# Kernel optimization log

Hardware: AMD Instinct MI355X
Metric: run time of the kernel (lower is better)

## Reference

```python
import jax, jax.numpy as jnp
import numpy as np

DIM, NH, WS, SS, MLP_RATIO = 192, 6, 8, 4, 4
EPS = 1e-5


def _rel_pos_index(ws):
    coords = np.stack(np.meshgrid(np.arange(ws), np.arange(ws), indexing='ij')).reshape(2, -1)
    rel = (coords[:, :, None] - coords[:, None, :]).transpose(1, 2, 0)
    rel[:, :, 0] += ws - 1
    rel[:, :, 1] += ws - 1
    rel[:, :, 0] *= 2 * ws - 1
    return rel.sum(-1)  # (ws*ws, ws*ws) int


def _attn_mask(hp, wp, ws, ss):
    img = np.zeros((hp, wp))
    slices = (slice(0, -ws), slice(-ws, -ss), slice(-ss, None))
    cnt = 0
    for hs in slices:
        for vs in slices:
            img[hs, vs] = cnt
            cnt += 1
    mw = img.reshape(hp // ws, ws, wp // ws, ws).transpose(0, 2, 1, 3).reshape(-1, ws * ws)
    am = mw[:, None, :] - mw[:, :, None]  # (nW, N, N)
    return jnp.asarray(np.where(am != 0, -100.0, 0.0).astype(np.float32))


def _ln(x, g, b):
    mu = jnp.mean(x, axis=-1, keepdims=True)
    var = jnp.mean(jnp.square(x - mu), axis=-1, keepdims=True)
    return (x - mu) * jax.lax.rsqrt(var + EPS) * g + b


def setup_inputs():
    key = jax.random.key(0)
    ks = jax.random.split(key, 8)
    B, H, W, C = 8, 128, 128, DIM
    hid = C * MLP_RATIO
    n = lambda k, s: jax.random.normal(k, s, dtype=jnp.float32) * 0.02
    return {
        'x': jax.random.normal(ks[0], (B, H * W, C), dtype=jnp.float32),
        'h': H, 'w': W,
        'norm1_g': jnp.ones((C,), jnp.float32), 'norm1_b': jnp.zeros((C,), jnp.float32),
        'qkv_w': n(ks[1], (C, 3 * C)), 'qkv_b': jnp.zeros((3 * C,), jnp.float32),
        'proj_w': n(ks[2], (C, C)), 'proj_b': jnp.zeros((C,), jnp.float32),
        'rel_bias_table': n(ks[3], ((2 * WS - 1) ** 2, NH)),
        'norm2_g': jnp.ones((C,), jnp.float32), 'norm2_b': jnp.zeros((C,), jnp.float32),
        'fc1_w': n(ks[4], (C, hid)), 'fc1_b': jnp.zeros((hid,), jnp.float32),
        'fc2_w': n(ks[5], (hid, C)), 'fc2_b': jnp.zeros((C,), jnp.float32),
    }


def reference(x, h, w, norm1_g, norm1_b, qkv_w, qkv_b, proj_w, proj_b,
              rel_bias_table, norm2_g, norm2_b, fc1_w, fc1_b, fc2_w, fc2_b):
    B, L, C = x.shape
    ws, ss, nh = WS, SS, NH
    hd = C // nh
    scale = hd ** (-0.5)

    shortcut = x
    xg = _ln(x, norm1_g, norm1_b).reshape(B, h, w, C)

    pad_h = (-h) % ws
    pad_w = (-w) % ws
    if pad_h or pad_w:
        xg = jnp.pad(xg, ((0, 0), (0, pad_h), (0, pad_w), (0, 0)))
    hp, wp = h + pad_h, w + pad_w
    if ss > 0:
        xg = jnp.roll(xg, (-ss, -ss), axis=(1, 2))

    # window partition -> (nB, N, C)
    win = xg.reshape(B, hp // ws, ws, wp // ws, ws, C).transpose(0, 1, 3, 2, 4, 5).reshape(-1, ws * ws, C)
    nB, N, _ = win.shape

    qkv = (win @ qkv_w + qkv_b).reshape(nB, N, 3, nh, hd).transpose(2, 0, 3, 1, 4)
    q, k, v = qkv[0] * scale, qkv[1], qkv[2]  # (nB, nh, N, hd)

    attn = jnp.einsum('bhnd,bhmd->bhnm', q, k)  # (nB, nh, N, N)
    rpi = _rel_pos_index(ws)
    bias = rel_bias_table[rpi.reshape(-1)].reshape(N, N, nh).transpose(2, 0, 1)
    attn = attn + bias[None]
    if ss > 0:
        mask = _attn_mask(hp, wp, ws, ss)  # (nW, N, N)
        nW = mask.shape[0]
        attn = (attn.reshape(nB // nW, nW, nh, N, N) + mask[None, :, None]).reshape(nB, nh, N, N)
    attn = jax.nn.softmax(attn, axis=-1)

    out = jnp.einsum('bhnm,bhmd->bnhd', attn, v).reshape(nB, N, C)
    out = out @ proj_w + proj_b

    # window reverse
    out = out.reshape(B, hp // ws, wp // ws, ws, ws, C).transpose(0, 1, 3, 2, 4, 5).reshape(B, hp, wp, C)
    if ss > 0:
        out = jnp.roll(out, (ss, ss), axis=(1, 2))
    out = out[:, :h, :w].reshape(B, h * w, C)

    x = shortcut + out
    xn2 = _ln(x, norm2_g, norm2_b)
    mlp = jax.nn.gelu(xn2 @ fc1_w + fc1_b, approximate=False) @ fc2_w + fc2_b
    return x + mlp
```

## Files before the change

kernel.cpp:

```cpp
#include <hip/hip_runtime.h>

typedef unsigned short u16;
typedef unsigned int   u32;
typedef __attribute__((ext_vector_type(8))) short bf16x8;
typedef __attribute__((ext_vector_type(4))) float f32x4;

#define L_TOK   16384
#define C_DIM   192
#define HID_DIM 768

#define OFF_QKV  0
#define OFF_PROJ 110592
#define OFF_FC1  147456
#define OFF_FC2  294912
#define CVT_TOT  442368

union FragU { int4 i4; bf16x8 h8; };

#define MFMA_B16(a,b,c) __builtin_amdgcn_mfma_f32_16x16x32_bf16(a,b,c,0,0,0)

__device__ __forceinline__ u16 f2bf(float f) {
    u32 t; __builtin_memcpy(&t, &f, 4);
    t += 0x7FFFu + ((t >> 16) & 1u);
    return (u16)(t >> 16);
}

__global__ __launch_bounds__(256) void k_cvt(
    const float* __restrict__ qkvw, const float* __restrict__ projw,
    const float* __restrict__ fc1w, const float* __restrict__ fc2w,
    u16* __restrict__ ws)
{
    const int i = blockIdx.x * 256 + threadIdx.x;
    if (i >= CVT_TOT) return;
    float v; int dst;
    if (i < OFF_PROJ) {
        const int k = i / 576, col = i % 576;
        const int grp = col / 192, rem = col % 192;
        const int head = rem >> 5, dim = rem & 31;
        v = qkvw[i];
        dst = OFF_QKV + head * (96 * 192) + (grp * 32 + dim) * 192 + k;
    } else if (i < OFF_FC1) {
        const int s = i - OFF_PROJ;
        const int cin = s / 192, cout = s % 192;
        const int head = cin >> 5, j = cin & 31;
        v = projw[s];
        dst = OFF_PROJ + head * (192 * 32) + cout * 32 + j;
    } else if (i < OFF_FC2) {
        const int s = i - OFF_FC1;
        const int k = s / 768, h = s % 768;
        v = fc1w[s];
        dst = OFF_FC1 + h * 192 + k;
    } else {
        const int s = i - OFF_FC2;
        const int h = s / 192, c = s % 192;
        v = fc2w[s];
        dst = OFF_FC2 + c * 768 + h;
    }
    ws[dst] = f2bf(v);
}

__global__ __launch_bounds__(256, 2) void k_attnproj(
    const float* __restrict__ x, const float* __restrict__ g1v, const float* __restrict__ b1v,
    const u16* __restrict__ qkvwT, const float* __restrict__ qkvb,
    const float* __restrict__ relb, const u16* __restrict__ projT, const float* __restrict__ projb,
    float* __restrict__ x1)
{
    struct PW {
        u16 qsb[64 * 40];
        u16 ksb[64 * 40];
        u16 vsbT[32 * 72];
        u16 psb[64 * 72];
        u16 oh [64 * 40];
    };
    union SmemU {
        u16 xw[128 * 200];
        PW pw[2];
    };
    __shared__ __align__(16) SmemU u;
    __shared__ __align__(16) u16 wbuf[192 * 40];
    __shared__ float relbs[225 * 6];

    const int t  = threadIdx.x;
    const int lane = t & 63, w = t >> 6;
    const int win = w >> 1, half = w & 1;
    const int l15 = lane & 15, quad = lane >> 4;
    const int wi2 = blockIdx.x * 2 + win;
    const int b  = wi2 >> 8;
    const int hb = (wi2 >> 4) & 15;
    const int wb = wi2 & 15;
    const bool maskon = (hb == 15) || (wb == 15);
    const f32x4 zf = {0.f, 0.f, 0.f, 0.f};

    for (int i = t; i < 225 * 6; i += 256) relbs[i] = relb[i];

    #pragma unroll
    for (int tk = 0; tk < 2; ++tk) {
        const int nn = t >> 2, q4 = t & 3;
        const int tok = tk * 64 + nn;
        const int tw = tok >> 6, n = tok & 63;
        const int wiA = blockIdx.x * 2 + tw;
        const int bA  = wiA >> 8;
        const int hbA = (wiA >> 4) & 15, wbA = wiA & 15;
        const int r = n >> 3, c = n & 7;
        const int ho = (hbA * 8 + r + 4) & 127;
        const int wo = (wbA * 8 + c + 4) & 127;
        const size_t xoff = ((size_t)bA * L_TOK + ho * 128 + wo) * C_DIM;
        const float* xp = x + xoff + q4 * 48;
        float f[48];
        float sum = 0.f, sq = 0.f;
        #pragma unroll
        for (int i = 0; i < 12; ++i) {
            float4 v = *(const float4*)(xp + i * 4);
            f[i*4+0]=v.x; f[i*4+1]=v.y; f[i*4+2]=v.z; f[i*4+3]=v.w;
            sum += v.x+v.y+v.z+v.w;
            sq  += v.x*v.x + v.y*v.y + v.z*v.z + v.w*v.w;
        }
        sum += __shfl_xor(sum, 1); sum += __shfl_xor(sum, 2);
        sq  += __shfl_xor(sq, 1);  sq  += __shfl_xor(sq, 2);
        const float mu = sum * (1.f / 192.f);
        const float rstd = rsqrtf(sq * (1.f / 192.f) - mu * mu + 1e-5f);
        u16* xrow = u.xw + tok * 200 + q4 * 48;
        #pragma unroll
        for (int i = 0; i < 6; ++i) {
            u32 pk[4];
            #pragma unroll
            for (int j = 0; j < 4; ++j) {
                float g0 = g1v[q4*48 + i*8 + j*2],     b0 = b1v[q4*48 + i*8 + j*2];
                float g1 = g1v[q4*48 + i*8 + j*2 + 1], b1 = b1v[q4*48 + i*8 + j*2 + 1];
                float y0 = (f[i*8+j*2]   - mu) * rstd * g0 + b0;
                float y1 = (f[i*8+j*2+1] - mu) * rstd * g1 + b1;
                pk[j] = (u32)f2bf(y0) | (((u32)f2bf(y1)) << 16);
            }
            *(int4*)(xrow + i * 8) = make_int4((int)pk[0], (int)pk[1], (int)pk[2], (int)pk[3]);
        }
    }
    __syncthreads();

    FragU afrag[2][6];
    #pragma unroll
    for (int mt = 0; mt < 2; ++mt)
        #pragma unroll
        for (int kk = 0; kk < 6; ++kk)
            afrag[mt][kk].i4 = *(const int4*)(u.xw +
                (win*64 + half*32 + mt*16 + l15) * 200 + kk*32 + quad*8);

    PW* P = &u.pw[win];
    const int rb = half*32 + quad*4;

    f32x4 acc2[2][12];
    #pragma unroll
    for (int mt = 0; mt < 2; ++mt)
        #pragma unroll
        for (int nt = 0; nt < 12; ++nt) acc2[mt][nt] = zf;

    for (int head = 0; head < 6; ++head) {
        f32x4 accq[2][6];
        #pragma unroll
        for (int mt = 0; mt < 2; ++mt)
            #pragma unroll
            for (int nt = 0; nt < 6; ++nt) accq[mt][nt] = zf;

        for (int kc = 0; kc < 3; ++kc) {
            __syncthreads();
            {
                const u16* src = qkvwT + (size_t)head * (96 * 192) + kc * 64;
                #pragma unroll
                for (int i = 0; i < 3; ++i) {
                    const int e = t + i * 256;
                    const int cc = e >> 3, seg = e & 7;
                    *(int4*)(wbuf + cc*72 + seg*8) =
                        *(const int4*)(src + cc*192 + seg*8);
                }
            }
            __syncthreads();
            #pragma unroll
            for (int s = 0; s < 2; ++s) {
                #pragma unroll
                for (int nt = 0; nt < 6; ++nt) {
                    FragU bf_;
                    bf_.i4 = *(const int4*)(wbuf + (nt*16 + l15)*72 + s*32 + quad*8);
                    accq[0][nt] = MFMA_B16(afrag[0][kc*2 + s].h8, bf_.h8, accq[0][nt]);
                    accq[1][nt] = MFMA_B16(afrag[1][kc*2 + s].h8, bf_.h8, accq[1][nt]);
                }
            }
        }
        #pragma unroll
        for (int mt = 0; mt < 2; ++mt) {
            #pragma unroll
            for (int nt = 0; nt < 6; ++nt) {
                const int grp = nt >> 1;
                const int dim = (nt & 1)*16 + l15;
                const float bias = qkvb[grp*192 + head*32 + dim];
                float vv[4];
                #pragma unroll
                for (int rg = 0; rg < 4; ++rg) vv[rg] = accq[mt][nt][rg] + bias;
                const int rowb = rb + mt*16;
                if (grp == 0) {
                    #pragma unroll
                    for (int rg = 0; rg < 4; ++rg)
                        P->qsb[(rowb + rg)*40 + dim] = f2bf(vv[rg] * 0.17677669529663687f);
                } else if (grp == 1) {
                    #pragma unroll
                    for (int rg = 0; rg < 4; ++rg)
                        P->ksb[(rowb + rg)*40 + dim] = f2bf(vv[rg]);
                } else {
                    u32 lo = (u32)f2bf(vv[0]) | (((u32)f2bf(vv[1])) << 16);
                    u32 hi = (u32)f2bf(vv[2]) | (((u32)f2bf(vv[3])) << 16);
                    *(uint2*)&P->vsbT[dim*72 + rowb] = make_uint2(lo, hi);
                }
            }
        }
        __syncthreads();

        FragU qf0, qf1;
        qf0.i4 = *(const int4*)(P->qsb + (half*32 + l15)*40 + quad*8);
        qf1.i4 = *(const int4*)(P->qsb + (half*32 + 16 + l15)*40 + quad*8);
        f32x4 sv[2][4];
        #pragma unroll
        for (int nt = 0; nt < 4; ++nt) {
            FragU kf; kf.i4 = *(const int4*)(P->ksb + (nt*16 + l15)*40 + quad*8);
            sv[0][nt] = MFMA_B16(qf0.h8, kf.h8, zf);
            sv[1][nt] = MFMA_B16(qf1.h8, kf.h8, zf);
        }
        const int kr_ = l15 >> 3, kc2 = l15 & 7;
        #pragma unroll
        for (int mt = 0; mt < 2; ++mt) {
            #pragma unroll
            for (int rg = 0; rg < 4; ++rg) {
                const int qm = rb + mt*16 + rg;
                const int qr = qm >> 3, qc = qm & 7;
                #pragma unroll
                for (int nt = 0; nt < 4; ++nt) {
                    const int kr = nt*2 + kr_;
                    sv[mt][nt][rg] += relbs[((qr - kr + 7)*15 + (qc - kc2 + 7))*6 + head];
                }
            }
        }
        if (maskon) {
            #pragma unroll
            for (int mt = 0; mt < 2; ++mt) {
                #pragma unroll
                for (int rg = 0; rg < 4; ++rg) {
                    const int qm = rb + mt*16 + rg;
                    const int qr = qm >> 3, qc = qm & 7;
                    const int regq = ((hb == 15) ? (qr < 4 ? 1 : 2) : 0) * 3
                                   + ((wb == 15) ? (qc < 4 ? 1 : 2) : 0);
                    #pragma unroll
                    for (int nt = 0; nt < 4; ++nt) {
                        const int kr = nt*2 + kr_;
                        const int regk = ((hb == 15) ? (kr < 4 ? 1 : 2) : 0) * 3
                                       + ((wb == 15) ? (kc2 < 4 ? 1 : 2) : 0);
                        if (regq != regk) sv[mt][nt][rg] -= 100.f;
                    }
                }
            }
        }
        #pragma unroll
        for (int mt = 0; mt < 2; ++mt) {
            #pragma unroll
            for (int rg = 0; rg < 4; ++rg) {
                float mx = fmaxf(fmaxf(sv[mt][0][rg], sv[mt][1][rg]),
                                 fmaxf(sv[mt][2][rg], sv[mt][3][rg]));
                mx = fmaxf(mx, __shfl_xor(mx, 1));
                mx = fmaxf(mx, __shfl_xor(mx, 2));
                mx = fmaxf(mx, __shfl_xor(mx, 4));
                mx = fmaxf(mx, __shfl_xor(mx, 8));
                float s0 = 0.f;
                #pragma unroll
                for (int nt = 0; nt < 4; ++nt) {
                    sv[mt][nt][rg] = __expf(sv[mt][nt][rg] - mx); s0 += sv[mt][nt][rg];
                }
                s0 += __shfl_xor(s0, 1); s0 += __shfl_xor(s0, 2);
                s0 += __shfl_xor(s0, 4); s0 += __shfl_xor(s0, 8);
                const float inv = 1.f / s0;
                #pragma unroll
                for (int nt = 0; nt < 4; ++nt)
                    P->psb[(rb + mt*16 + rg)*72 + nt*16 + l15] = f2bf(sv[mt][nt][rg] * inv);
            }
        }

        FragU vb[2][2];
        #pragma unroll
        for (int ntv = 0; ntv < 2; ++ntv) {
            vb[ntv][0].i4 = *(const int4*)(P->vsbT + (ntv*16 + l15)*72 + quad*8);
            vb[ntv][1].i4 = *(const int4*)(P->vsbT + (ntv*16 + l15)*72 + 32 + quad*8);
        }
        #pragma unroll
        for (int mt = 0; mt < 2; ++mt) {
            FragU pa0, pa1;
            pa0.i4 = *(const int4*)(P->psb + (half*32 + mt*16 + l15)*72 + quad*8);
            pa1.i4 = *(const int4*)(P->psb + (half*32 + mt*16 + l15)*72 + 32 + quad*8);
            f32x4 ov0 = zf, ov1 = zf;
            ov0 = MFMA_B16(pa0.h8, vb[0][0].h8, ov0);
            ov0 = MFMA_B16(pa1.h8, vb[0][1].h8, ov0);
            ov1 = MFMA_B16(pa0.h8, vb[1][0].h8, ov1);
            ov1 = MFMA_B16(pa1.h8, vb[1][1].h8, ov1);
            #pragma unroll
            for (int rg = 0; rg < 4; ++rg) {
                P->oh[(rb + mt*16 + rg)*40 + l15]      = f2bf(ov0[rg]);
                P->oh[(rb + mt*16 + rg)*40 + 16 + l15] = f2bf(ov1[rg]);
            }
        }

        {
            const u16* src = projT + (size_t)head * (192 * 32);
            #pragma unroll
            for (int i = 0; i < 3; ++i) {
                const int e = t + i * 256;
                const int c = e >> 2, seg = e & 3;
                *(int4*)(wbuf + c*40 + seg*8) =
                    *(const int4*)(src + c*32 + seg*8);
            }
        }
        __syncthreads();
        FragU ao0, ao1;
        ao0.i4 = *(const int4*)(P->oh + (half*32 + l15)*40 + quad*8);
        ao1.i4 = *(const int4*)(P->oh + (half*32 + 16 + l15)*40 + quad*8);
        #pragma unroll
        for (int nt = 0; nt < 12; ++nt) {
            FragU bp; bp.i4 = *(const int4*)(wbuf + (nt*16 + l15)*40 + quad*8);
            acc2[0][nt] = MFMA_B16(ao0.h8, bp.h8, acc2[0][nt]);
            acc2[1][nt] = MFMA_B16(ao1.h8, bp.h8, acc2[1][nt]);
        }
    }

    {
        float pb[12];
        #pragma unroll
        for (int nt = 0; nt < 12; ++nt) pb[nt] = projb[nt*16 + l15];
        #pragma unroll
        for (int mt = 0; mt < 2; ++mt) {
            #pragma unroll
            for (int rg = 0; rg < 4; ++rg) {
                const int tok = rb + mt*16 + rg;
                const int tr = tok >> 3, tc = tok & 7;
                const int ho2 = (hb * 8 + tr + 4) & 127;
                const int wo2 = (wb * 8 + tc + 4) & 127;
                const size_t base = ((size_t)b * L_TOK + ho2 * 128 + wo2) * C_DIM;
                #pragma unroll
                for (int nt = 0; nt < 12; ++nt) {
                    const int col = nt*16 + l15;
                    x1[base + col] = acc2[mt][nt][rg] + pb[nt] + x[base + col];
                }
            }
        }
    }
}

__global__ __launch_bounds__(256, 2) void k_mlp(
    const float* x1, const float* __restrict__ g2v, const float* __restrict__ b2v,
    const u16* __restrict__ fc1wT, const float* __restrict__ fc1b,
    const u16* __restrict__ fc2wT, const float* __restrict__ fc2b,
    float* out)
{
    union SmemU {
        u16 xn[128 * 200];
        struct {
            u16 wT[192 * 40];
            u16 hbuf[128 * 104];
        } s;
    };
    __shared__ __align__(16) SmemU u;

    const int blk = blockIdx.x;
    const int t = threadIdx.x;
    const size_t row0 = (size_t)blk * 128;
    const int lane = t & 63, w = t >> 6;
    const int l15 = lane & 15, quad = lane >> 4;
    const f32x4 zf = {0.f, 0.f, 0.f, 0.f};

    #pragma unroll
    for (int tk = 0; tk < 2; ++tk) {
        const int nn = t >> 2, q4 = t & 3;
        const int tok = tk * 64 + nn;
        const float* xp = x1 + (row0 + tok) * C_DIM + q4 * 48;
        float f[48];
        float sum = 0.f, sq = 0.f;
        #pragma unroll
        for (int i = 0; i < 12; ++i) {
            float4 v = *(const float4*)(xp + i * 4);
            f[i*4+0]=v.x; f[i*4+1]=v.y; f[i*4+2]=v.z; f[i*4+3]=v.w;
            sum += v.x+v.y+v.z+v.w;
            sq  += v.x*v.x + v.y*v.y + v.z*v.z + v.w*v.w;
        }
        sum += __shfl_xor(sum,1); sum += __shfl_xor(sum,2);
        sq  += __shfl_xor(sq,1);  sq  += __shfl_xor(sq,2);
        const float mu = sum * (1.f/192.f);
        const float rstd = rsqrtf(sq * (1.f/192.f) - mu*mu + 1e-5f);
        u16* xrow = u.xn + tok * 200 + q4 * 48;
        #pragma unroll
        for (int i = 0; i < 6; ++i) {
            u32 pk[4];
            #pragma unroll
            for (int j = 0; j < 4; ++j) {
                float g0 = g2v[q4*48 + i*8 + j*2],     b0 = b2v[q4*48 + i*8 + j*2];
                float g1 = g2v[q4*48 + i*8 + j*2 + 1], b1 = b2v[q4*48 + i*8 + j*2 + 1];
                float y0 = (f[i*8+j*2]   - mu) * rstd * g0 + b0;
                float y1 = (f[i*8+j*2+1] - mu) * rstd * g1 + b1;
                pk[j] = (u32)f2bf(y0) | (((u32)f2bf(y1)) << 16);
            }
            *(int4*)(xrow + i*8) = make_int4((int)pk[0], (int)pk[1], (int)pk[2], (int)pk[3]);
        }
    }
    __syncthreads();

    FragU afrag[2][6];
    #pragma unroll
    for (int mt = 0; mt < 2; ++mt)
        #pragma unroll
        for (int kk = 0; kk < 6; ++kk)
            afrag[mt][kk].i4 = *(const int4*)(u.xn + (mt*64 + w*16 + l15) * 200 + kk*32 + quad*8);

    f32x4 acc2[2][12];
    #pragma unroll
    for (int mt = 0; mt < 2; ++mt)
        #pragma unroll
        for (int nt = 0; nt < 12; ++nt) acc2[mt][nt] = zf;

    for (int hc = 0; hc < 8; ++hc) {
        f32x4 acc1[2][6];
        #pragma unroll
        for (int mt = 0; mt < 2; ++mt)
            #pragma unroll
            for (int nt = 0; nt < 6; ++nt) acc1[mt][nt] = zf;

        for (int kc = 0; kc < 3; ++kc) {
            __syncthreads();
            {
                const u16* src = fc1wT + (size_t)(hc * 96) * 192 + kc * 64;
                #pragma unroll
                for (int i = 0; i < 3; ++i) {
                    const int e = t + i * 256;
                    const int cc = e >> 3, seg = e & 7;
                    *(int4*)(u.s.wT + cc*72 + seg*8) =
                        *(const int4*)(src + cc*192 + seg*8);
                }
            }
            __syncthreads();
            #pragma unroll
            for (int s = 0; s < 2; ++s) {
                #pragma unroll
                for (int nt = 0; nt < 6; ++nt) {
                    FragU bf_;
                    bf_.i4 = *(const int4*)(u.s.wT + (nt*16 + l15)*72 + s*32 + quad*8);
                    acc1[0][nt] = MFMA_B16(afrag[0][kc*2 + s].h8, bf_.h8, acc1[0][nt]);
                    acc1[1][nt] = MFMA_B16(afrag[1][kc*2 + s].h8, bf_.h8, acc1[1][nt]);
                }
            }
        }
        #pragma unroll
        for (int nt = 0; nt < 6; ++nt) {
            const float bb = fc1b[hc*96 + nt*16 + l15];
            #pragma unroll
            for (int mt = 0; mt < 2; ++mt) {
                #pragma unroll
                for (int rg = 0; rg < 4; ++rg) {
                    float h = acc1[mt][nt][rg] + bb;
                    float g = 0.5f * h * (1.f + erff(h * 0.70710678118654752f));
                    u.s.hbuf[(mt*64 + w*16 + quad*4 + rg) * 104 + nt*16 + l15] = f2bf(g);
                }
            }
        }
        for (int sc = 0; sc < 3; ++sc) {
            __syncthreads();
            {
                const u16* src = fc2wT + hc * 96 + sc * 32;
                #pragma unroll
                for (int i = 0; i < 3; ++i) {
                    const int e = t + i * 256;
                    const int c = e >> 2, seg = e & 3;
                    *(int4*)(u.s.wT + c*40 + seg*8) =
                        *(const int4*)(src + c*768 + seg*8);
                }
            }
            __syncthreads();
            FragU ha0, ha1;
            ha0.i4 = *(const int4*)(u.s.hbuf + (w*16 + l15) * 104 + sc*32 + quad*8);
            ha1.i4 = *(const int4*)(u.s.hbuf + (64 + w*16 + l15) * 104 + sc*32 + quad*8);
            #pragma unroll
            for (int nt = 0; nt < 12; ++nt) {
                FragU bf_;
                bf_.i4 = *(const int4*)(u.s.wT + (nt*16 + l15)*40 + quad*8);
                acc2[0][nt] = MFMA_B16(ha0.h8, bf_.h8, acc2[0][nt]);
                acc2[1][nt] = MFMA_B16(ha1.h8, bf_.h8, acc2[1][nt]);
            }
        }
    }

    #pragma unroll
    for (int nt = 0; nt < 12; ++nt) {
        const int col = nt*16 + l15;
        const float bb = fc2b[col];
        #pragma unroll
        for (int mt = 0; mt < 2; ++mt) {
            #pragma unroll
            for (int rg = 0; rg < 4; ++rg) {
                const size_t idx = (row0 + mt*64 + w*16 + quad*4 + rg) * C_DIM + col;
                out[idx] = acc2[mt][nt][rg] + bb + x1[idx];
            }
        }
    }
}

extern "C" void kernel_launch(void* const* d_in, const int* in_sizes, int n_in,
                              void* d_out, int out_size, void* d_ws, size_t ws_size,
                              hipStream_t stream) {
    const float* x     = (const float*)d_in[0];
    const float* g1v   = (const float*)d_in[3];
    const float* b1v   = (const float*)d_in[4];
    const float* qkvw  = (const float*)d_in[5];
    const float* qkvb  = (const float*)d_in[6];
    const float* projw = (const float*)d_in[7];
    const float* projb = (const float*)d_in[8];
    const float* relb  = (const float*)d_in[9];
    const float* g2v   = (const float*)d_in[10];
    const float* b2v   = (const float*)d_in[11];
    const float* fc1w  = (const float*)d_in[12];
    const float* fc1b  = (const float*)d_in[13];
    const float* fc2w  = (const float*)d_in[14];
    const float* fc2b  = (const float*)d_in[15];

    float* x1 = (float*)d_out;
    u16* wsb  = (u16*)d_ws;

    hipLaunchKernelGGL(k_cvt, dim3((CVT_TOT + 255) / 256), dim3(256), 0, stream,
                       qkvw, projw, fc1w, fc2w, wsb);
    hipLaunchKernelGGL(k_attnproj, dim3(1024), dim3(256), 0, stream,
                       x, g1v, b1v, wsb + OFF_QKV, qkvb, relb, wsb + OFF_PROJ, projb, x1);
    hipLaunchKernelGGL(k_mlp, dim3(1024), dim3(256), 0, stream,
                       x1, g2v, b2v, wsb + OFF_FC1, fc1b, wsb + OFF_FC2, fc2b, x1);
}
```

Baseline: 563.7 us.

## Prefetch next weight tile into registers while computing current tile

Both the attention and MLP kernels now issue the global loads for the next weight chunk (qkv/proj, fc1/fc2) into registers right after the barrier, overlapping their latency with the current MFMA work, then store them to shared memory at the next step. In the MLP kernel the weight buffer is moved out of the union so it no longer aliases the LN output buffer while the prefetch pipeline runs. This adds 12 VGPRs of staging per thread and slightly more shared memory, which could reduce occupancy under launch_bounds(256,2).

Result: faster. 535.6 us (-5.0%).

```diff
diff --git a/kernel.cpp b/kernel.cpp
--- a/kernel.cpp
+++ b/kernel.cpp
@@ -147,6 +147,33 @@
     PW* P = &u.pw[win];
     const int rb = half*32 + quad*4;
 
+    int4 wr0, wr1, wr2;
+    auto LOADW = [&](int hh, int sub) {
+        if (sub < 3) {
+            const u16* src = qkvwT + (size_t)hh * (96 * 192) + sub * 64;
+            wr0 = *(const int4*)(src + ((t      ) >> 3) * 192 + ((t      ) & 7) * 8);
+            wr1 = *(const int4*)(src + ((t + 256) >> 3) * 192 + ((t + 256) & 7) * 8);
+            wr2 = *(const int4*)(src + ((t + 512) >> 3) * 192 + ((t + 512) & 7) * 8);
+        } else {
+            const u16* src = projT + (size_t)hh * (192 * 32);
+            wr0 = *(const int4*)(src + ((t      ) >> 2) * 32 + ((t      ) & 3) * 8);
+            wr1 = *(const int4*)(src + ((t + 256) >> 2) * 32 + ((t + 256) & 3) * 8);
+            wr2 = *(const int4*)(src + ((t + 512) >> 2) * 32 + ((t + 512) & 3) * 8);
+        }
+    };
+    auto STOREW = [&](int sub) {
+        if (sub < 3) {
+            *(int4*)(wbuf + ((t      ) >> 3) * 72 + ((t      ) & 7) * 8) = wr0;
+            *(int4*)(wbuf + ((t + 256) >> 3) * 72 + ((t + 256) & 7) * 8) = wr1;
+            *(int4*)(wbuf + ((t + 512) >> 3) * 72 + ((t + 512) & 7) * 8) = wr2;
+        } else {
+            *(int4*)(wbuf + ((t      ) >> 2) * 40 + ((t      ) & 3) * 8) = wr0;
+            *(int4*)(wbuf + ((t + 256) >> 2) * 40 + ((t + 256) & 3) * 8) = wr1;
+            *(int4*)(wbuf + ((t + 512) >> 2) * 40 + ((t + 512) & 3) * 8) = wr2;
+        }
+    };
+    LOADW(0, 0);
+
     f32x4 acc2[2][12];
     #pragma unroll
     for (int mt = 0; mt < 2; ++mt)
@@ -162,17 +189,9 @@
 
         for (int kc = 0; kc < 3; ++kc) {
             __syncthreads();
-            {
-                const u16* src = qkvwT + (size_t)head * (96 * 192) + kc * 64;
-                #pragma unroll
-                for (int i = 0; i < 3; ++i) {
-                    const int e = t + i * 256;
-                    const int cc = e >> 3, seg = e & 7;
-                    *(int4*)(wbuf + cc*72 + seg*8) =
-                        *(const int4*)(src + cc*192 + seg*8);
-                }
-            }
+            STOREW(kc);
             __syncthreads();
+            LOADW(head, kc + 1);
             #pragma unroll
             for (int s = 0; s < 2; ++s) {
                 #pragma unroll
@@ -302,17 +321,9 @@
             }
         }
 
-        {
-            const u16* src = projT + (size_t)head * (192 * 32);
-            #pragma unroll
-            for (int i = 0; i < 3; ++i) {
-                const int e = t + i * 256;
-                const int c = e >> 2, seg = e & 3;
-                *(int4*)(wbuf + c*40 + seg*8) =
-                    *(const int4*)(src + c*32 + seg*8);
-            }
-        }
+        STOREW(3);
         __syncthreads();
+        if (head < 5) LOADW(head + 1, 0);
         FragU ao0, ao1;
         ao0.i4 = *(const int4*)(P->oh + (half*32 + l15)*40 + quad*8);
         ao1.i4 = *(const int4*)(P->oh + (half*32 + 16 + l15)*40 + quad*8);
@@ -355,12 +366,10 @@
 {
     union SmemU {
         u16 xn[128 * 200];
-        struct {
-            u16 wT[192 * 40];
-            u16 hbuf[128 * 104];
-        } s;
+        u16 hbuf[128 * 104];
     };
     __shared__ __align__(16) SmemU u;
+    __shared__ __align__(16) u16 wT[192 * 40];
 
     const int blk = blockIdx.x;
     const int t = threadIdx.x;
@@ -411,6 +420,33 @@
         for (int kk = 0; kk < 6; ++kk)
             afrag[mt][kk].i4 = *(const int4*)(u.xn + (mt*64 + w*16 + l15) * 200 + kk*32 + quad*8);
 
+    int4 wr0, wr1, wr2;
+    auto LOADW = [&](int hcL, int sub) {
+        if (sub < 3) {
+            const u16* src = fc1wT + (size_t)(hcL * 96) * 192 + sub * 64;
+            wr0 = *(const int4*)(src + ((t      ) >> 3) * 192 + ((t      ) & 7) * 8);
+            wr1 = *(const int4*)(src + ((t + 256) >> 3) * 192 + ((t + 256) & 7) * 8);
+            wr2 = *(const int4*)(src + ((t + 512) >> 3) * 192 + ((t + 512) & 7) * 8);
+        } else {
+            const u16* src = fc2wT + hcL * 96 + (sub - 3) * 32;
+            wr0 = *(const int4*)(src + ((t      ) >> 2) * 768 + ((t      ) & 3) * 8);
+            wr1 = *(const int4*)(src + ((t + 256) >> 2) * 768 + ((t + 256) & 3) * 8);
+            wr2 = *(const int4*)(src + ((t + 512) >> 2) * 768 + ((t + 512) & 3) * 8);
+        }
+    };
+    auto STOREW = [&](int sub) {
+        if (sub < 3) {
+            *(int4*)(wT + ((t      ) >> 3) * 72 + ((t      ) & 7) * 8) = wr0;
+            *(int4*)(wT + ((t + 256) >> 3) * 72 + ((t + 256) & 7) * 8) = wr1;
+            *(int4*)(wT + ((t + 512) >> 3) * 72 + ((t + 512) & 7) * 8) = wr2;
+        } else {
+            *(int4*)(wT + ((t      ) >> 2) * 40 + ((t      ) & 3) * 8) = wr0;
+            *(int4*)(wT + ((t + 256) >> 2) * 40 + ((t + 256) & 3) * 8) = wr1;
+            *(int4*)(wT + ((t + 512) >> 2) * 40 + ((t + 512) & 3) * 8) = wr2;
+        }
+    };
+    LOADW(0, 0);
+
     f32x4 acc2[2][12];
     #pragma unroll
     for (int mt = 0; mt < 2; ++mt)
@@ -426,23 +462,15 @@
 
         for (int kc = 0; kc < 3; ++kc) {
             __syncthreads();
-            {
-                const u16* src = fc1wT + (size_t)(hc * 96) * 192 + kc * 64;
-                #pragma unroll
-                for (int i = 0; i < 3; ++i) {
-                    const int e = t + i * 256;
-                    const int cc = e >> 3, seg = e & 7;
-                    *(int4*)(u.s.wT + cc*72 + seg*8) =
-                        *(const int4*)(src + cc*192 + seg*8);
-                }
-            }
+            STOREW(kc);
             __syncthreads();
+            LOADW(hc, kc + 1);
             #pragma unroll
             for (int s = 0; s < 2; ++s) {
                 #pragma unroll
                 for (int nt = 0; nt < 6; ++nt) {
                     FragU bf_;
-                    bf_.i4 = *(const int4*)(u.s.wT + (nt*16 + l15)*72 + s*32 + quad*8);
+                    bf_.i4 = *(const int4*)(wT + (nt*16 + l15)*72 + s*32 + quad*8);
                     acc1[0][nt] = MFMA_B16(afrag[0][kc*2 + s].h8, bf_.h8, acc1[0][nt]);
                     acc1[1][nt] = MFMA_B16(afrag[1][kc*2 + s].h8, bf_.h8, acc1[1][nt]);
                 }
@@ -457,30 +485,23 @@
                 for (int rg = 0; rg < 4; ++rg) {
                     float h = acc1[mt][nt][rg] + bb;
                     float g = 0.5f * h * (1.f + erff(h * 0.70710678118654752f));
-                    u.s.hbuf[(mt*64 + w*16 + quad*4 + rg) * 104 + nt*16 + l15] = f2bf(g);
+                    u.hbuf[(mt*64 + w*16 + quad*4 + rg) * 104 + nt*16 + l15] = f2bf(g);
                 }
             }
         }
         for (int sc = 0; sc < 3; ++sc) {
             __syncthreads();
-            {
-                const u16* src = fc2wT + hc * 96 + sc * 32;
-                #pragma unroll
-                for (int i = 0; i < 3; ++i) {
-                    const int e = t + i * 256;
-                    const int c = e >> 2, seg = e & 3;
-                    *(int4*)(u.s.wT + c*40 + seg*8) =
-                        *(const int4*)(src + c*768 + seg*8);
-                }
-            }
+            STOREW(3 + sc);
             __syncthreads();
+            if (sc < 2)           LOADW(hc, 4 + sc);
+            else if (hc < 7)      LOADW(hc + 1, 0);
             FragU ha0, ha1;
-            ha0.i4 = *(const int4*)(u.s.hbuf + (w*16 + l15) * 104 + sc*32 + quad*8);
-            ha1.i4 = *(const int4*)(u.s.hbuf + (64 + w*16 + l15) * 104 + sc*32 + quad*8);
+            ha0.i4 = *(const int4*)(u.hbuf + (w*16 + l15) * 104 + sc*32 + quad*8);
+            ha1.i4 = *(const int4*)(u.hbuf + (64 + w*16 + l15) * 104 + sc*32 + quad*8);
             #pragma unroll
             for (int nt = 0; nt < 12; ++nt) {
                 FragU bf_;
-                bf_.i4 = *(const int4*)(u.s.wT + (nt*16 + l15)*40 + quad*8);
+                bf_.i4 = *(const int4*)(wT + (nt*16 + l15)*40 + quad*8);
                 acc2[0][nt] = MFMA_B16(ha0.h8, bf_.h8, acc2[0][nt]);
                 acc2[1][nt] = MFMA_B16(ha1.h8, bf_.h8, acc2[1][nt]);
             }
```

## Load weight MFMA fragments directly from global instead of staging in LDS

Applied to the files above, without the earlier changes.

Both the attention/projection kernel and the MLP kernel now read the QKV, proj, fc1 and fc2 weight B-fragments straight from global memory into registers. This replaces the cooperative copy into a shared weight buffer and drops the paired barriers around every K chunk. The weight buffer is removed from shared memory, which shrinks the LDS footprint and could allow more resident blocks. The cost is that every wave issues its own, redundant global loads, relying on L1/L2 hits, and that load latency sits right in front of the MFMAs because the loops are not unrolled. The removed barriers may also weaken the ordering of LDS reuse across heads.

After: 796.8 us. +41.4%, slower.

```diff
diff --git a/kernel.cpp b/kernel.cpp
--- a/kernel.cpp
+++ b/kernel.cpp
@@ -77,7 +77,6 @@
         PW pw[2];
     };
     __shared__ __align__(16) SmemU u;
-    __shared__ __align__(16) u16 wbuf[192 * 40];
     __shared__ float relbs[225 * 6];
 
     const int t  = threadIdx.x;
@@ -143,6 +142,7 @@
         for (int kk = 0; kk < 6; ++kk)
             afrag[mt][kk].i4 = *(const int4*)(u.xw +
                 (win*64 + half*32 + mt*16 + l15) * 200 + kk*32 + quad*8);
+    __syncthreads();
 
     PW* P = &u.pw[win];
     const int rb = half*32 + quad*4;
@@ -154,33 +154,25 @@
         for (int nt = 0; nt < 12; ++nt) acc2[mt][nt] = zf;
 
     for (int head = 0; head < 6; ++head) {
+        const u16* qwb = qkvwT + (size_t)head * (96 * 192) + l15 * 192 + quad * 8;
         f32x4 accq[2][6];
         #pragma unroll
         for (int mt = 0; mt < 2; ++mt)
             #pragma unroll
             for (int nt = 0; nt < 6; ++nt) accq[mt][nt] = zf;
 
+        #pragma unroll 1
         for (int kc = 0; kc < 3; ++kc) {
-            __syncthreads();
-            {
-                const u16* src = qkvwT + (size_t)head * (96 * 192) + kc * 64;
-                #pragma unroll
-                for (int i = 0; i < 3; ++i) {
-                    const int e = t + i * 256;
-                    const int cc = e >> 3, seg = e & 7;
-                    *(int4*)(wbuf + cc*72 + seg*8) =
-                        *(const int4*)(src + cc*192 + seg*8);
-                }
-            }
-            __syncthreads();
             #pragma unroll
             for (int s = 0; s < 2; ++s) {
+                FragU bf_[6];
+                #pragma unroll
+                for (int nt = 0; nt < 6; ++nt)
+                    bf_[nt].i4 = *(const int4*)(qwb + nt*(16*192) + kc*64 + s*32);
                 #pragma unroll
                 for (int nt = 0; nt < 6; ++nt) {
-                    FragU bf_;
-                    bf_.i4 = *(const int4*)(wbuf + (nt*16 + l15)*72 + s*32 + quad*8);
-                    accq[0][nt] = MFMA_B16(afrag[0][kc*2 + s].h8, bf_.h8, accq[0][nt]);
-                    accq[1][nt] = MFMA_B16(afrag[1][kc*2 + s].h8, bf_.h8, accq[1][nt]);
+                    accq[0][nt] = MFMA_B16(afrag[0][kc*2 + s].h8, bf_[nt].h8, accq[0][nt]);
+                    accq[1][nt] = MFMA_B16(afrag[1][kc*2 + s].h8, bf_[nt].h8, accq[1][nt]);
                 }
             }
         }
@@ -301,24 +293,15 @@
                 P->oh[(rb + mt*16 + rg)*40 + 16 + l15] = f2bf(ov1[rg]);
             }
         }
-
-        {
-            const u16* src = projT + (size_t)head * (192 * 32);
-            #pragma unroll
-            for (int i = 0; i < 3; ++i) {
-                const int e = t + i * 256;
-                const int c = e >> 2, seg = e & 3;
-                *(int4*)(wbuf + c*40 + seg*8) =
-                    *(const int4*)(src + c*32 + seg*8);
-            }
-        }
         __syncthreads();
+
+        const u16* pwb = projT + (size_t)head * (192 * 32) + l15 * 32 + quad * 8;
         FragU ao0, ao1;
         ao0.i4 = *(const int4*)(P->oh + (half*32 + l15)*40 + quad*8);
         ao1.i4 = *(const int4*)(P->oh + (half*32 + 16 + l15)*40 + quad*8);
         #pragma unroll
         for (int nt = 0; nt < 12; ++nt) {
-            FragU bp; bp.i4 = *(const int4*)(wbuf + (nt*16 + l15)*40 + quad*8);
+            FragU bp; bp.i4 = *(const int4*)(pwb + nt*(16*32));
             acc2[0][nt] = MFMA_B16(ao0.h8, bp.h8, acc2[0][nt]);
             acc2[1][nt] = MFMA_B16(ao1.h8, bp.h8, acc2[1][nt]);
         }
@@ -355,10 +338,7 @@
 {
     union SmemU {
         u16 xn[128 * 200];
-        struct {
-            u16 wT[192 * 40];
-            u16 hbuf[128 * 104];
-        } s;
+        u16 hbuf[128 * 104];
     };
     __shared__ __align__(16) SmemU u;
 
@@ -410,6 +390,7 @@
         #pragma unroll
         for (int kk = 0; kk < 6; ++kk)
             afrag[mt][kk].i4 = *(const int4*)(u.xn + (mt*64 + w*16 + l15) * 200 + kk*32 + quad*8);
+    __syncthreads();
 
     f32x4 acc2[2][12];
     #pragma unroll
@@ -417,6 +398,10 @@
         #pragma unroll
         for (int nt = 0; nt < 12; ++nt) acc2[mt][nt] = zf;
 
+    const u16* w1b = fc1wT + (size_t)l15 * 192 + quad * 8;
+    const u16* w2b = fc2wT + (size_t)l15 * 768 + quad * 8;
+
+    #pragma unroll 1
     for (int hc = 0; hc < 8; ++hc) {
         f32x4 acc1[2][6];
         #pragma unroll
@@ -424,27 +409,19 @@
             #pragma unroll
             for (int nt = 0; nt < 6; ++nt) acc1[mt][nt] = zf;
 
+        const u16* w1h = w1b + (size_t)(hc * 96) * 192;
+        #pragma unroll 1
         for (int kc = 0; kc < 3; ++kc) {
-            __syncthreads();
-            {
-                const u16* src = fc1wT + (size_t)(hc * 96) * 192 + kc * 64;
-                #pragma unroll
-                for (int i = 0; i < 3; ++i) {
-                    const int e = t + i * 256;
-                    const int cc = e >> 3, seg = e & 7;
-                    *(int4*)(u.s.wT + cc*72 + seg*8) =
-                        *(const int4*)(src + cc*192 + seg*8);
-                }
-            }
-            __syncthreads();
             #pragma unroll
             for (int s = 0; s < 2; ++s) {
+                FragU bf_[6];
+                #pragma unroll
+                for (int nt = 0; nt < 6; ++nt)
+                    bf_[nt].i4 = *(const int4*)(w1h + nt*(16*192) + kc*64 + s*32);
                 #pragma unroll
                 for (int nt = 0; nt < 6; ++nt) {
-                    FragU bf_;
-                    bf_.i4 = *(const int4*)(u.s.wT + (nt*16 + l15)*72 + s*32 + quad*8);
-                    acc1[0][nt] = MFMA_B16(afrag[0][kc*2 + s].h8, bf_.h8, acc1[0][nt]);
-                    acc1[1][nt] = MFMA_B16(afrag[1][kc*2 + s].h8, bf_.h8, acc1[1][nt]);
+                    acc1[0][nt] = MFMA_B16(afrag[0][kc*2 + s].h8, bf_[nt].h8, acc1[0][nt]);
+                    acc1[1][nt] = MFMA_B16(afrag[1][kc*2 + s].h8, bf_[nt].h8, acc1[1][nt]);
                 }
             }
         }
@@ -457,32 +434,23 @@
                 for (int rg = 0; rg < 4; ++rg) {
                     float h = acc1[mt][nt][rg] + bb;
                     float g = 0.5f * h * (1.f + erff(h * 0.70710678118654752f));
-                    u.s.hbuf[(mt*64 + w*16 + quad*4 + rg) * 104 + nt*16 + l15] = f2bf(g);
-                }
-            }
-        }
+                    u.hbuf[(mt*64 + w*16 + quad*4 + rg) * 104 + nt*16 + l15] = f2bf(g);
+                }
+            }
+        }
+        #pragma unroll 1
         for (int sc = 0; sc < 3; ++sc) {
-            __syncthreads();
-            {
-                const u16* src = fc2wT + hc * 96 + sc * 32;
-                #pragma unroll
-                for (int i = 0; i < 3; ++i) {
-                    const int e = t + i * 256;
-                    const int c = e >> 2, seg = e & 3;
-                    *(int4*)(u.s.wT + c*40 + seg*8) =
-                        *(const int4*)(src + c*768 + seg*8);
-                }
-            }
-            __syncthreads();
             FragU ha0, ha1;
-            ha0.i4 = *(const int4*)(u.s.hbuf + (w*16 + l15) * 104 + sc*32 + quad*8);
-            ha1.i4 = *(const int4*)(u.s.hbuf + (64 + w*16 + l15) * 104 + sc*32 + quad*8);
+            ha0.i4 = *(const int4*)(u.hbuf + (w*16 + l15) * 104 + sc*32 + quad*8);
+            ha1.i4 = *(const int4*)(u.hbuf + (64 + w*16 + l15) * 104 + sc*32 + quad*8);
+            FragU bf_[12];
+            #pragma unroll
+            for (int nt = 0; nt < 12; ++nt)
+                bf_[nt].i4 = *(const int4*)(w2b + (size_t)nt*(16*768) + hc*96 + sc*32);
             #pragma unroll
             for (int nt = 0; nt < 12; ++nt) {
-                FragU bf_;
-                bf_.i4 = *(const int4*)(u.s.wT + (nt*16 + l15)*40 + quad*8);
-                acc2[0][nt] = MFMA_B16(ha0.h8, bf_.h8, acc2[0][nt]);
-                acc2[1][nt] = MFMA_B16(ha1.h8, bf_.h8, acc2[1][nt]);
+                acc2[0][nt] = MFMA_B16(ha0.h8, bf_[nt].h8, acc2[0][nt]);
+                acc2[1][nt] = MFMA_B16(ha1.h8, bf_[nt].h8, acc2[1][nt]);
             }
         }
     }
```
